# Kernel optimization log

Hardware: AMD Instinct MI355X
Metric: run time of the kernel (lower is better)

## Reference

```python
import jax, jax.numpy as jnp
import numpy as np

B, S, D, H, DFF = 1, 2048, 4096, 16, 16384
HD = D // H
EPS = 1e-5


def layernorm(x, w, b):
    mu = jnp.mean(x, axis=-1, keepdims=True)
    var = jnp.mean(jnp.square(x - mu), axis=-1, keepdims=True)
    return (x - mu) * jax.lax.rsqrt(var + EPS) * w + b


def setup_inputs() -> dict:
    key = jax.random.key(0)
    ks = jax.random.split(key, 5)
    inv = lambda n: 1.0 / np.sqrt(n)
    return {
        "hidden_states": jax.random.normal(ks[0], (B, S, D), jnp.float32),
        "ln1_w": jnp.ones((D,), jnp.float32),
        "ln1_b": jnp.zeros((D,), jnp.float32),
        "ln2_w": jnp.ones((D,), jnp.float32),
        "ln2_b": jnp.zeros((D,), jnp.float32),
        "w_qkv": jax.random.normal(ks[1], (D, 3 * D), jnp.float32) * inv(D),
        "b_qkv": jnp.zeros((3 * D,), jnp.float32),
        "w_dense": jax.random.normal(ks[2], (D, D), jnp.float32) * inv(D),
        "b_dense": jnp.zeros((D,), jnp.float32),
        "w_fc1": jax.random.normal(ks[3], (D, DFF), jnp.float32) * inv(D),
        "b_fc1": jnp.zeros((DFF,), jnp.float32),
        "w_fc2": jax.random.normal(ks[4], (DFF, D), jnp.float32) * inv(DFF),
        "b_fc2": jnp.zeros((D,), jnp.float32),
    }


def _attention(x, w_qkv, b_qkv, w_dense, b_dense):
    qkv = x @ w_qkv + b_qkv                      # [B,S,3D]
    q, k, v = jnp.split(qkv, 3, axis=-1)
    q = q.reshape(B, S, H, HD)
    k = k.reshape(B, S, H, HD)
    v = v.reshape(B, S, H, HD)
    scale = HD ** (-0.5)
    scores = jnp.einsum("bqhd,bkhd->bhqk", q, k) * scale
    causal = jnp.tril(jnp.ones((S, S), bool))
    scores = jnp.where(causal, scores, jnp.float32(-1e30))
    probs = jax.nn.softmax(scores, axis=-1)
    out = jnp.einsum("bhqk,bkhd->bqhd", probs, v).reshape(B, S, D)
    return out @ w_dense + b_dense


def _mlp(x, w_fc1, b_fc1, w_fc2, b_fc2):
    h = jax.nn.gelu(x @ w_fc1 + b_fc1, approximate=True)  # gelu_new (tanh)
    return h @ w_fc2 + b_fc2


def reference(hidden_states, ln1_w, ln1_b, ln2_w, ln2_b, w_qkv, b_qkv,
              w_dense, b_dense, w_fc1, b_fc1, w_fc2, b_fc2):
    attn_in = layernorm(hidden_states, ln1_w, ln1_b)
    attn_out = _attention(attn_in, w_qkv, b_qkv, w_dense, b_dense)
    # use_parallel_residual = True
    mlp_in = layernorm(hidden_states, ln2_w, ln2_b)
    mlp_out = _mlp(mlp_in, w_fc1, b_fc1, w_fc2, b_fc2)
    return mlp_out + attn_out + hidden_states
```

## Files before the change

### kernel.cpp

```cpp
#include <hip/hip_runtime.h>
#include <cstdint>
#include <cstddef>

typedef __bf16 bf16;
typedef __bf16 bf16x8 __attribute__((ext_vector_type(8)));
typedef float f32x4 __attribute__((ext_vector_type(4)));

#define SEQ 2048
#define DIM 4096
#define NHEAD 16
#define HDIM 256
#define DFF_N 16384
#define D3 12288

__global__ __launch_bounds__(256) void ln_kernel(
    const float* __restrict__ x,
    const float* __restrict__ w1, const float* __restrict__ b1,
    const float* __restrict__ w2, const float* __restrict__ b2,
    bf16* __restrict__ x1, bf16* __restrict__ x2)
{
  int row = blockIdx.x;
  int t = threadIdx.x;
  const float* xr = x + (size_t)row * DIM + t * 16;
  float v[16];
  float s = 0.f, sq = 0.f;
#pragma unroll
  for (int i = 0; i < 4; i++) {
    float4 f = ((const float4*)xr)[i];
    v[i*4+0] = f.x; v[i*4+1] = f.y; v[i*4+2] = f.z; v[i*4+3] = f.w;
  }
#pragma unroll
  for (int i = 0; i < 16; i++) { s += v[i]; sq += v[i]*v[i]; }
#pragma unroll
  for (int o = 32; o; o >>= 1) { s += __shfl_xor(s, o, 64); sq += __shfl_xor(sq, o, 64); }
  __shared__ float rs[4], rq[4];
  int wave = t >> 6, lane = t & 63;
  if (lane == 0) { rs[wave] = s; rq[wave] = sq; }
  __syncthreads();
  s  = rs[0] + rs[1] + rs[2] + rs[3];
  sq = rq[0] + rq[1] + rq[2] + rq[3];
  float mean = s * (1.f/DIM);
  float var  = sq * (1.f/DIM) - mean*mean;
  float rstd = rsqrtf(var + 1e-5f);
  int c0 = t*16;
#pragma unroll
  for (int i = 0; i < 16; i++) {
    int c = c0 + i;
    float nv = (v[i] - mean) * rstd;
    x1[(size_t)row*DIM + c] = (bf16)(nv * w1[c] + b1[c]);
    x2[(size_t)row*DIM + c] = (bf16)(nv * w2[c] + b2[c]);
  }
}

template <int EPI>
__global__ __launch_bounds__(256) void gemm_kernel(
    const bf16* __restrict__ A, const float* __restrict__ B,
    const float* __restrict__ bias,
    const float* __restrict__ add1, const float* __restrict__ add2,
    void* __restrict__ Cout, int M, int N, int K)
{
  __shared__ __align__(16) bf16 As[128][40];
  __shared__ float Bs[32][129];
  const int t = threadIdx.x;
  const int lane = t & 63;
  const int wave = t >> 6;
  const int l15 = lane & 15, l4 = lane >> 4;
  const int m0 = blockIdx.x * 128;
  const int n0 = blockIdx.y * 128;
  const int wm = (wave >> 1) * 64;
  const int wn = (wave & 1) * 64;

  f32x4 acc[4][4];
#pragma unroll
  for (int i = 0; i < 4; i++)
#pragma unroll
    for (int j = 0; j < 4; j++) acc[i][j] = (f32x4){0.f, 0.f, 0.f, 0.f};

  for (int k0 = 0; k0 < K; k0 += 32) {
#pragma unroll
    for (int i = 0; i < 2; i++) {
      int c = t + i * 256;
      int row = c >> 2, seg = c & 3;
      *(bf16x8*)&As[row][seg * 8] =
          *(const bf16x8*)(A + (size_t)(m0 + row) * K + k0 + seg * 8);
    }
#pragma unroll
    for (int i = 0; i < 4; i++) {
      int c = t + i * 256;
      int kr = c >> 5, ns = c & 31;
      float4 bv = *(const float4*)(B + (size_t)(k0 + kr) * N + n0 + ns * 4);
      Bs[kr][ns*4+0] = bv.x; Bs[kr][ns*4+1] = bv.y;
      Bs[kr][ns*4+2] = bv.z; Bs[kr][ns*4+3] = bv.w;
    }
    __syncthreads();

    bf16x8 af[4];
#pragma unroll
    for (int mi = 0; mi < 4; mi++)
      af[mi] = *(const bf16x8*)&As[wm + mi * 16 + l15][l4 * 8];
#pragma unroll
    for (int ni = 0; ni < 4; ni++) {
      bf16x8 bfv;
#pragma unroll
      for (int j = 0; j < 8; j++)
        bfv[j] = (bf16)Bs[l4 * 8 + j][wn + ni * 16 + l15];
#pragma unroll
      for (int mi = 0; mi < 4; mi++)
        acc[mi][ni] = __builtin_amdgcn_mfma_f32_16x16x32_bf16(af[mi], bfv, acc[mi][ni], 0, 0, 0);
    }
    __syncthreads();
  }

#pragma unroll
  for (int mi = 0; mi < 4; mi++) {
#pragma unroll
    for (int ni = 0; ni < 4; ni++) {
#pragma unroll
      for (int r = 0; r < 4; r++) {
        int m = m0 + wm + mi * 16 + l4 * 4 + r;
        int n = n0 + wn + ni * 16 + l15;
        size_t idx = (size_t)m * N + n;
        float val = acc[mi][ni][r] + bias[n];
        if (EPI == 0) {
          ((bf16*)Cout)[idx] = (bf16)val;
        } else if (EPI == 1) {
          ((float*)Cout)[idx] = val;
        } else if (EPI == 2) {
          float u = 0.7978845608028654f * (val + 0.044715f * val * val * val);
          float e = __expf(2.f * u);
          float th = 1.f - 2.f / (e + 1.f);
          ((bf16*)Cout)[idx] = (bf16)(0.5f * val * (1.f + th));
        } else {
          ((float*)Cout)[idx] = val + add1[idx] + add2[idx];
        }
      }
    }
  }
}

__global__ __launch_bounds__(256) void attn_kernel(
    const bf16* __restrict__ qkv, bf16* __restrict__ attn)
{
  extern __shared__ float smem[];
  float (*sc)[2049] = (float (*)[2049])smem;
  float* inv = smem + 16 * 2049;

  const int qt = blockIdx.x;
  const int h  = blockIdx.y;
  const int q0 = qt * 16;
  const int t = threadIdx.x;
  const int lane = t & 63, w = t >> 6;
  const int l15 = lane & 15, l4 = lane >> 4;

  bf16x8 qf[8];
  {
    const bf16* qbase = qkv + (size_t)(q0 + l15) * D3 + h * HDIM + l4 * 8;
#pragma unroll
    for (int dt = 0; dt < 8; dt++)
      qf[dt] = *(const bf16x8*)(qbase + dt * 32);
  }

  for (int kt = w; kt <= qt; kt += 4) {
    int k0 = kt * 16;
    f32x4 a = (f32x4){0.f, 0.f, 0.f, 0.f};
    const bf16* kbase = qkv + (size_t)(k0 + l15) * D3 + DIM + h * HDIM + l4 * 8;
#pragma unroll
    for (int dt = 0; dt < 8; dt++) {
      bf16x8 kf = *(const bf16x8*)(kbase + dt * 32);
      a = __builtin_amdgcn_mfma_f32_16x16x32_bf16(qf[dt], kf, a, 0, 0, 0);
    }
#pragma unroll
    for (int r = 0; r < 4; r++) {
      int qrow = l4 * 4 + r;
      int kcol = k0 + l15;
      float sv = a[r] * 0.0625f;
      if (kcol > q0 + qrow) sv = -1e30f;
      sc[qrow][kcol] = sv;
    }
  }
  __syncthreads();

  const int nk = q0 + 16;
  const int row = w * 4 + l4;
  float mx = -1e38f;
  for (int c = l15; c < nk; c += 16) mx = fmaxf(mx, sc[row][c]);
#pragma unroll
  for (int o = 8; o; o >>= 1) mx = fmaxf(mx, __shfl_xor(mx, o, 64));
  float sum = 0.f;
  for (int c = l15; c < nk; c += 16) {
    float e = __expf(sc[row][c] - mx);
    sc[row][c] = e;
    sum += e;
  }
#pragma unroll
  for (int o = 8; o; o >>= 1) sum += __shfl_xor(sum, o, 64);
  if (l15 == 0) inv[row] = 1.f / sum;
  if (!(qt & 1)) sc[row][nk + l15] = 0.f;
  __syncthreads();

  f32x4 o_acc[4];
#pragma unroll
  for (int i = 0; i < 4; i++) o_acc[i] = (f32x4){0.f, 0.f, 0.f, 0.f};
  const int nchunks = (qt + 2) >> 1;
  for (int c32 = 0; c32 < nchunks; c32++) {
    int k0 = c32 * 32;
    bf16x8 pf;
#pragma unroll
    for (int j = 0; j < 8; j++)
      pf[j] = (bf16)sc[l15][k0 + l4 * 8 + j];
#pragma unroll
    for (int ni = 0; ni < 4; ni++) {
      bf16x8 vf;
#pragma unroll
      for (int j = 0; j < 8; j++)
        vf[j] = qkv[(size_t)(k0 + l4 * 8 + j) * D3 + 2 * DIM + h * HDIM + w * 64 + ni * 16 + l15];
      o_acc[ni] = __builtin_amdgcn_mfma_f32_16x16x32_bf16(pf, vf, o_acc[ni], 0, 0, 0);
    }
  }
#pragma unroll
  for (int ni = 0; ni < 4; ni++) {
#pragma unroll
    for (int r = 0; r < 4; r++) {
      int qrow = l4 * 4 + r;
      float val = o_acc[ni][r] * inv[qrow];
      attn[(size_t)(q0 + qrow) * DIM + h * HDIM + w * 64 + ni * 16 + l15] = (bf16)val;
    }
  }
}

extern "C" void kernel_launch(void* const* d_in, const int* in_sizes, int n_in,
                              void* d_out, int out_size, void* d_ws, size_t ws_size,
                              hipStream_t stream)
{
  const float* hidden  = (const float*)d_in[0];
  const float* ln1w    = (const float*)d_in[1];
  const float* ln1b    = (const float*)d_in[2];
  const float* ln2w    = (const float*)d_in[3];
  const float* ln2b    = (const float*)d_in[4];
  const float* w_qkv   = (const float*)d_in[5];
  const float* b_qkv   = (const float*)d_in[6];
  const float* w_dense = (const float*)d_in[7];
  const float* b_dense = (const float*)d_in[8];
  const float* w_fc1   = (const float*)d_in[9];
  const float* b_fc1   = (const float*)d_in[10];
  const float* w_fc2   = (const float*)d_in[11];
  const float* b_fc2   = (const float*)d_in[12];

  char* ws = (char*)d_ws;
  bf16* x1        = (bf16*)(ws);
  bf16* x2        = (bf16*)(ws + 16777216);
  bf16* qkv       = (bf16*)(ws + 33554432);
  bf16* attn      = (bf16*)(ws + 83886080);
  bf16* h1        = (bf16*)(ws + 100663296);
  float* dense_o  = (float*)(ws + 167772160);
  float* out      = (float*)d_out;

  hipFuncSetAttribute(reinterpret_cast<const void*>(attn_kernel),
                      hipFuncAttributeMaxDynamicSharedMemorySize, 131264);

  ln_kernel<<<SEQ, 256, 0, stream>>>(hidden, ln1w, ln1b, ln2w, ln2b, x1, x2);

  gemm_kernel<0><<<dim3(16, 96), 256, 0, stream>>>(
      x1, w_qkv, b_qkv, nullptr, nullptr, (void*)qkv, SEQ, D3, DIM);

  attn_kernel<<<dim3(SEQ / 16, NHEAD), 256, 131264, stream>>>(qkv, attn);

  gemm_kernel<1><<<dim3(16, 32), 256, 0, stream>>>(
      attn, w_dense, b_dense, nullptr, nullptr, (void*)dense_o, SEQ, DIM, DIM);

  gemm_kernel<2><<<dim3(16, 128), 256, 0, stream>>>(
      x2, w_fc1, b_fc1, nullptr, nullptr, (void*)h1, SEQ, DFF_N, DIM);

  gemm_kernel<3><<<dim3(16, 32), 256, 0, stream>>>(
      h1, w_fc2, b_fc2, dense_o, hidden, (void*)out, SEQ, DIM, DFF_N);
}
```

Baseline: 3.086 ms.

## Pre-transpose weights to bf16 and load GEMM tiles directly into LDS

Adds a transpose kernel that converts each fp32 weight matrix into a K-contiguous bf16 copy before its GEMM. The GEMM can then load both operands with global_load_lds 16-byte copies and read B fragments as vectors, instead of loading fp32 B, converting per element and doing strided LDS reads. The MLP is split into two halves to fit a smaller workspace, with the second FC2 half accumulating into the output, and a tile-index swizzle is added for L2 locality. This costs extra transpose passes over every weight on each call.

```diff
diff --git a/kernel.cpp b/kernel.cpp
--- a/kernel.cpp
+++ b/kernel.cpp
@@ -12,6 +12,7 @@
 #define HDIM 256
 #define DFF_N 16384
 #define D3 12288
+#define DHALF 8192
 
 __global__ __launch_bounds__(256) void ln_kernel(
     const float* __restrict__ x,
@@ -52,21 +53,56 @@
   }
 }
 
+__global__ __launch_bounds__(256) void transpose_kernel(
+    const float* __restrict__ in, bf16* __restrict__ out,
+    int ldin, int k0, int n0, int ldout)
+{
+  __shared__ float tile[64][65];
+  const int t = threadIdx.x;
+  const int kb = k0 + blockIdx.x * 64;
+  const int nb = n0 + blockIdx.y * 64;
+#pragma unroll
+  for (int i = 0; i < 4; i++) {
+    int c = t + i * 256;
+    int r = c >> 4, c4 = (c & 15) * 4;
+    float4 v = *(const float4*)(in + (size_t)(kb + r) * ldin + nb + c4);
+    tile[r][c4+0] = v.x; tile[r][c4+1] = v.y;
+    tile[r][c4+2] = v.z; tile[r][c4+3] = v.w;
+  }
+  __syncthreads();
+#pragma unroll
+  for (int i = 0; i < 2; i++) {
+    int c = t + i * 256;
+    int n = c >> 3, k8 = (c & 7) * 8;
+    bf16x8 o;
+#pragma unroll
+    for (int j = 0; j < 8; j++) o[j] = (bf16)tile[k8 + j][n];
+    *(bf16x8*)(out + (size_t)(blockIdx.y * 64 + n) * ldout + blockIdx.x * 64 + k8) = o;
+  }
+}
+
 template <int EPI>
 __global__ __launch_bounds__(256) void gemm_kernel(
-    const bf16* __restrict__ A, const float* __restrict__ B,
+    const bf16* __restrict__ A, const bf16* __restrict__ BT,
     const float* __restrict__ bias,
     const float* __restrict__ add1, const float* __restrict__ add2,
     void* __restrict__ Cout, int M, int N, int K)
 {
-  __shared__ __align__(16) bf16 As[128][40];
-  __shared__ float Bs[32][129];
+  __shared__ __align__(16) bf16 As[128 * 32];
+  __shared__ __align__(16) bf16 Bs[128 * 32];
   const int t = threadIdx.x;
   const int lane = t & 63;
   const int wave = t >> 6;
   const int l15 = lane & 15, l4 = lane >> 4;
-  const int m0 = blockIdx.x * 128;
-  const int n0 = blockIdx.y * 128;
+
+  const int nwgx = gridDim.x;
+  const int nwg = nwgx * gridDim.y;
+  const int orig = blockIdx.y * nwgx + blockIdx.x;
+  const int cpx = nwg >> 3;
+  const int swz = (orig & 7) * cpx + (orig >> 3);
+  const int m0 = (swz % nwgx) * 128;
+  const int n0 = (swz / nwgx) * 128;
+
   const int wm = (wave >> 1) * 64;
   const int wn = (wave & 1) * 64;
 
@@ -76,38 +112,34 @@
 #pragma unroll
     for (int j = 0; j < 4; j++) acc[i][j] = (f32x4){0.f, 0.f, 0.f, 0.f};
 
+  const bf16* Abase = A + (size_t)m0 * K;
+  const bf16* Bbase = BT + (size_t)n0 * K;
   for (int k0 = 0; k0 < K; k0 += 32) {
 #pragma unroll
     for (int i = 0; i < 2; i++) {
       int c = t + i * 256;
-      int row = c >> 2, seg = c & 3;
-      *(bf16x8*)&As[row][seg * 8] =
-          *(const bf16x8*)(A + (size_t)(m0 + row) * K + k0 + seg * 8);
-    }
-#pragma unroll
-    for (int i = 0; i < 4; i++) {
-      int c = t + i * 256;
-      int kr = c >> 5, ns = c & 31;
-      float4 bv = *(const float4*)(B + (size_t)(k0 + kr) * N + n0 + ns * 4);
-      Bs[kr][ns*4+0] = bv.x; Bs[kr][ns*4+1] = bv.y;
-      Bs[kr][ns*4+2] = bv.z; Bs[kr][ns*4+3] = bv.w;
+      int row = c >> 2, seg = (c & 3) * 8;
+      __builtin_amdgcn_global_load_lds(
+          (const __attribute__((address_space(1))) void*)(Abase + (size_t)row * K + k0 + seg),
+          (__attribute__((address_space(3))) void*)(As + c * 8), 16, 0, 0);
+      __builtin_amdgcn_global_load_lds(
+          (const __attribute__((address_space(1))) void*)(Bbase + (size_t)row * K + k0 + seg),
+          (__attribute__((address_space(3))) void*)(Bs + c * 8), 16, 0, 0);
     }
     __syncthreads();
 
-    bf16x8 af[4];
+    bf16x8 af[4], bfv[4];
 #pragma unroll
     for (int mi = 0; mi < 4; mi++)
-      af[mi] = *(const bf16x8*)&As[wm + mi * 16 + l15][l4 * 8];
-#pragma unroll
-    for (int ni = 0; ni < 4; ni++) {
-      bf16x8 bfv;
-#pragma unroll
-      for (int j = 0; j < 8; j++)
-        bfv[j] = (bf16)Bs[l4 * 8 + j][wn + ni * 16 + l15];
+      af[mi] = *(const bf16x8*)(As + (wm + mi * 16 + l15) * 32 + l4 * 8);
+#pragma unroll
+    for (int ni = 0; ni < 4; ni++)
+      bfv[ni] = *(const bf16x8*)(Bs + (wn + ni * 16 + l15) * 32 + l4 * 8);
+#pragma unroll
+    for (int ni = 0; ni < 4; ni++)
 #pragma unroll
       for (int mi = 0; mi < 4; mi++)
-        acc[mi][ni] = __builtin_amdgcn_mfma_f32_16x16x32_bf16(af[mi], bfv, acc[mi][ni], 0, 0, 0);
-    }
+        acc[mi][ni] = __builtin_amdgcn_mfma_f32_16x16x32_bf16(af[mi], bfv[ni], acc[mi][ni], 0, 0, 0);
     __syncthreads();
   }
 
@@ -120,18 +152,21 @@
         int m = m0 + wm + mi * 16 + l4 * 4 + r;
         int n = n0 + wn + ni * 16 + l15;
         size_t idx = (size_t)m * N + n;
-        float val = acc[mi][ni][r] + bias[n];
+        float val = acc[mi][ni][r];
         if (EPI == 0) {
-          ((bf16*)Cout)[idx] = (bf16)val;
+          ((bf16*)Cout)[idx] = (bf16)(val + bias[n]);
         } else if (EPI == 1) {
-          ((float*)Cout)[idx] = val;
+          ((float*)Cout)[idx] = val + bias[n];
         } else if (EPI == 2) {
-          float u = 0.7978845608028654f * (val + 0.044715f * val * val * val);
+          float g = val + bias[n];
+          float u = 0.7978845608028654f * (g + 0.044715f * g * g * g);
           float e = __expf(2.f * u);
           float th = 1.f - 2.f / (e + 1.f);
-          ((bf16*)Cout)[idx] = (bf16)(0.5f * val * (1.f + th));
+          ((bf16*)Cout)[idx] = (bf16)(0.5f * g * (1.f + th));
+        } else if (EPI == 3) {
+          ((float*)Cout)[idx] = val + bias[n] + add1[idx] + add2[idx];
         } else {
-          ((float*)Cout)[idx] = val + add1[idx] + add2[idx];
+          ((float*)Cout)[idx] += val;
         }
       }
     }
@@ -247,30 +282,44 @@
   const float* b_fc2   = (const float*)d_in[12];
 
   char* ws = (char*)d_ws;
-  bf16* x1        = (bf16*)(ws);
-  bf16* x2        = (bf16*)(ws + 16777216);
-  bf16* qkv       = (bf16*)(ws + 33554432);
-  bf16* attn      = (bf16*)(ws + 83886080);
-  bf16* h1        = (bf16*)(ws + 100663296);
-  float* dense_o  = (float*)(ws + 167772160);
-  float* out      = (float*)d_out;
+  bf16*  wT      = (bf16*)(ws);
+  bf16*  h1      = (bf16*)(ws + 67108864);
+  bf16*  x1      = (bf16*)(ws + 100663296);
+  bf16*  attn    = (bf16*)(ws + 100663296);
+  bf16*  x2      = (bf16*)(ws + 117440512);
+  bf16*  qkv     = (bf16*)(ws + 134217728);
+  float* dense_o = (float*)(ws + 150994944);
+  float* out     = (float*)d_out;
 
   hipFuncSetAttribute(reinterpret_cast<const void*>(attn_kernel),
                       hipFuncAttributeMaxDynamicSharedMemorySize, 131264);
 
   ln_kernel<<<SEQ, 256, 0, stream>>>(hidden, ln1w, ln1b, ln2w, ln2b, x1, x2);
 
+  transpose_kernel<<<dim3(DIM/64, D3/64), 256, 0, stream>>>(w_qkv, wT, D3, 0, 0, DIM);
   gemm_kernel<0><<<dim3(16, 96), 256, 0, stream>>>(
-      x1, w_qkv, b_qkv, nullptr, nullptr, (void*)qkv, SEQ, D3, DIM);
+      x1, wT, b_qkv, nullptr, nullptr, (void*)qkv, SEQ, D3, DIM);
+
+  transpose_kernel<<<dim3(DIM/64, DIM/64), 256, 0, stream>>>(w_dense, wT, DIM, 0, 0, DIM);
 
   attn_kernel<<<dim3(SEQ / 16, NHEAD), 256, 131264, stream>>>(qkv, attn);
 
   gemm_kernel<1><<<dim3(16, 32), 256, 0, stream>>>(
-      attn, w_dense, b_dense, nullptr, nullptr, (void*)dense_o, SEQ, DIM, DIM);
-
-  gemm_kernel<2><<<dim3(16, 128), 256, 0, stream>>>(
-      x2, w_fc1, b_fc1, nullptr, nullptr, (void*)h1, SEQ, DFF_N, DIM);
-
-  gemm_kernel<3><<<dim3(16, 32), 256, 0, stream>>>(
-      h1, w_fc2, b_fc2, dense_o, hidden, (void*)out, SEQ, DIM, DFF_N);
-}
+      attn, wT, b_dense, nullptr, nullptr, (void*)dense_o, SEQ, DIM, DIM);
+
+  for (int hf = 0; hf < 2; hf++) {
+    transpose_kernel<<<dim3(DIM/64, DHALF/64), 256, 0, stream>>>(
+        w_fc1, wT, DFF_N, 0, hf * DHALF, DIM);
+    gemm_kernel<2><<<dim3(16, 64), 256, 0, stream>>>(
+        x2, wT, b_fc1 + hf * DHALF, nullptr, nullptr, (void*)h1, SEQ, DHALF, DIM);
+    transpose_kernel<<<dim3(DHALF/64, DIM/64), 256, 0, stream>>>(
+        w_fc2, wT, DIM, hf * DHALF, 0, DHALF);
+    if (hf == 0) {
+      gemm_kernel<3><<<dim3(16, 32), 256, 0, stream>>>(
+          h1, wT, b_fc2, dense_o, hidden, (void*)out, SEQ, DIM, DHALF);
+    } else {
+      gemm_kernel<4><<<dim3(16, 32), 256, 0, stream>>>(
+          h1, wT, nullptr, nullptr, nullptr, (void*)out, SEQ, DIM, DHALF);
+    }
+  }
+}
```

New measurement: 2.521 ms. 1.22x faster.
